# Optimization experiments

Measured on AMD Instinct MI355X. Metric: run time of the kernel, lower is better.

The kernel has to match this reference:

```python
import jax, jax.numpy as jnp
import numpy as np

NU = 100000
NV = 100000
EF = 500000
EB = 500000
D = 64  # e_in = u_in = v_in = e_out = 64; u_out = v_out = 64 -> nu_dim = nv_dim = 32
DC = D + D  # concat dim: node_in + e_in = 128


def _lin(key, din, dout):
    kw, kb = jax.random.split(key)
    lim = 1.0 / np.sqrt(din)
    W = jax.random.uniform(kw, (din, dout), jnp.float32, -lim, lim)
    b = jax.random.uniform(kb, (dout,), jnp.float32, -lim, lim)
    return W, b


def setup_inputs() -> dict:
    key = jax.random.key(0)
    ks = jax.random.split(key, 20)
    inp = {
        'f_feat': jax.random.normal(ks[0], (EF, D), jnp.float32),
        'b_feat': jax.random.normal(ks[1], (EB, D), jnp.float32),
        'u_feat': jax.random.normal(ks[2], (NU, D), jnp.float32),
        'v_feat': jax.random.normal(ks[3], (NV, D), jnp.float32),
        'fsrc': jax.random.randint(ks[4], (EF,), 0, NU, jnp.int32),
        'fdst': jax.random.randint(ks[5], (EF,), 0, NV, jnp.int32),
        'bsrc': jax.random.randint(ks[6], (EB,), 0, NV, jnp.int32),
        'bdst': jax.random.randint(ks[7], (EB,), 0, NU, jnp.int32),
    }
    inp['We'], inp['be'] = _lin(ks[8], D, D)        # e_linear
    inp['Wul'], inp['bul'] = _lin(ks[9], D, D)      # u_linear
    inp['Wvl'], inp['bvl'] = _lin(ks[10], D, D)     # v_linear
    inp['Wau'], inp['bau'] = _lin(ks[11], D, DC)    # W_ATTN_u: u_in -> v_in+e_in
    inp['Wav'], inp['bav'] = _lin(ks[12], D, DC)    # W_ATTN_v: v_in -> u_in+e_in
    inp['Wwu'], inp['bwu'] = _lin(ks[13], DC, D // 2)  # W_u
    inp['Wwv'], inp['bwv'] = _lin(ks[14], DC, D // 2)  # W_v
    inp['WVu'], inp['bVu'] = _lin(ks[15], D, D - D // 2)  # Vu
    inp['WVv'], inp['bVv'] = _lin(ks[16], D, D - D // 2)  # Vv
    return inp


def _edge_softmax(scores, dst, n):
    # scores: [E,1]; softmax over edges grouped by destination node
    m = jax.ops.segment_max(scores, dst, num_segments=n)
    e = jnp.exp(scores - m[dst])
    s = jax.ops.segment_sum(e, dst, num_segments=n)
    return e / s[dst]


def reference(f_feat, b_feat, u_feat, v_feat, fsrc, fdst, bsrc, bdst,
              We, be, Wul, bul, Wvl, bvl, Wau, bau, Wav, bav,
              Wwu, bwu, Wwv, bwv, WVu, bVu, WVv, bVv):
    Nu, Nv = u_feat.shape[0], v_feat.shape[0]
    he_u = u_feat @ Wul + bul
    he_v = v_feat @ Wvl + bvl
    # edge hidden: he_e + he of incident u and v (activation is None, dropout 0)
    hf = f_feat @ We + be + he_u[fsrc] + he_v[fdst]   # forward: src=u, dst=v
    hb = b_feat @ We + be + he_v[bsrc] + he_u[bdst]   # backward: src=v, dst=u
    # concat raw src node feat with raw edge feat
    h_ue = jnp.concatenate([u_feat[fsrc], f_feat], axis=-1)  # [EF, DC]
    h_ve = jnp.concatenate([v_feat[bsrc], b_feat], axis=-1)  # [EB, DC]
    att_u = u_feat @ Wau + bau  # [Nu, DC]
    att_v = v_feat @ Wav + bav  # [Nv, DC]
    s_f = jnp.sum(h_ue * att_v[fdst], axis=-1, keepdims=True)  # e_dot_v
    s_b = jnp.sum(h_ve * att_u[bdst], axis=-1, keepdims=True)
    sfm_f = _edge_softmax(s_f, fdst, Nv)
    sfm_b = _edge_softmax(s_b, bdst, Nu)
    agg_v = jax.ops.segment_sum(h_ue * sfm_f, fdst, num_segments=Nv)
    agg_u = jax.ops.segment_sum(h_ve * sfm_b, bdst, num_segments=Nu)
    h_nu = agg_u @ Wwu + bwu
    h_nv = agg_v @ Wwv + bwv
    hu = jnp.concatenate([u_feat @ WVu + bVu, h_nu], axis=-1)
    hv = jnp.concatenate([v_feat @ WVv + bVv, h_nv], axis=-1)
    return hf, hb, hu, hv
```

## Files before the change

kernel.cpp:

```cpp
#include <hip/hip_runtime.h>
#include <hip/hip_bf16.h>
#include <cstdint>

typedef __attribute__((ext_vector_type(4))) float f32x4;
typedef __attribute__((ext_vector_type(8))) short bf16x8;

__device__ inline unsigned short f2bf(float f) {
    union { float f; unsigned u; } v; v.f = f;
    unsigned r = v.u + 0x7FFFu + ((v.u >> 16) & 1u);
    return (unsigned short)(r >> 16);
}
__device__ inline float bf2f(unsigned short h) {
    union { unsigned u; float f; } v; v.u = ((unsigned)h) << 16;
    return v.f;
}

__global__ void prep_kernel(
    const float* __restrict__ We,
    const float* __restrict__ Wul, const float* __restrict__ Wau, const float* __restrict__ WVu,
    const float* __restrict__ Wvl, const float* __restrict__ Wav, const float* __restrict__ WVv,
    const float* __restrict__ Wwu, const float* __restrict__ Wwv,
    const float* __restrict__ bul, const float* __restrict__ bau, const float* __restrict__ bVu,
    const float* __restrict__ bvl, const float* __restrict__ bav, const float* __restrict__ bVv,
    unsigned short* __restrict__ WeXf, unsigned short* __restrict__ WeXb,
    unsigned short* __restrict__ WnTu, unsigned short* __restrict__ WnTv,
    float* __restrict__ bcu, float* __restrict__ bcv)
{
    int tid0 = blockIdx.x * blockDim.x + threadIdx.x;
    int stride = gridDim.x * blockDim.x;
    for (int i = tid0; i < 176 * 64; i += stride) {
        int c = i >> 6, k = i & 63;
        float vf, vb;
        if (c < 64)       { vf = We[k * 64 + c];               vb = vf; }
        else if (c < 96)  { vf = Wwv[(64 + k) * 32 + (c - 64)]; vb = Wwu[(64 + k) * 32 + (c - 64)]; }
        else if (c < 160) { vf = Wav[(c - 96) * 128 + 64 + k];  vb = Wau[(c - 96) * 128 + 64 + k]; }
        else if (c == 160){ vf = bav[64 + k];                   vb = bau[64 + k]; }
        else              { vf = 0.f;                           vb = 0.f; }
        WeXf[i] = f2bf(vf);
        WeXb[i] = f2bf(vb);
    }
    for (int i = tid0; i < 208 * 64; i += stride) {
        int c = i >> 6, k = i & 63;
        float vu, vv;
        if (c < 64)       { vu = Wul[k * 64 + c];           vv = Wvl[k * 64 + c]; }
        else if (c < 128) { vu = Wav[(c - 64) * 128 + k];   vv = Wau[(c - 64) * 128 + k]; }
        else if (c < 160) { vu = WVu[k * 32 + (c - 128)];   vv = WVv[k * 32 + (c - 128)]; }
        else if (c < 192) { vu = Wwv[k * 32 + (c - 160)];   vv = Wwu[k * 32 + (c - 160)]; }
        else if (c == 192){ vu = bav[k];                    vv = bau[k]; }
        else              { vu = 0.f;                       vv = 0.f; }
        WnTu[i] = f2bf(vu);
        WnTv[i] = f2bf(vv);
    }
    for (int i = tid0; i < 208; i += stride) {
        float u = 0.f, v = 0.f;
        if (i < 64)                { u = bul[i];       v = bvl[i]; }
        else if (i >= 128 && i < 160) { u = bVu[i - 128]; v = bVv[i - 128]; }
        bcu[i] = u; bcv[i] = v;
    }
}

__global__ __launch_bounds__(256, 4) void node_pre_kernel(
    int nbU, int NU, int NV,
    const float* __restrict__ featU, const float* __restrict__ featV,
    const unsigned short* __restrict__ WTu, const unsigned short* __restrict__ WTv,
    const float* __restrict__ bcu, const float* __restrict__ bcv,
    unsigned short* __restrict__ heU, unsigned short* __restrict__ heV,
    unsigned short* __restrict__ ztU, unsigned short* __restrict__ ztV,
    unsigned short* __restrict__ nbfU, unsigned short* __restrict__ nbfV,
    float* __restrict__ outU, float* __restrict__ outV,
    float* __restrict__ projU, float* __restrict__ projV,
    float* __restrict__ sbU, float* __restrict__ sbV,
    float* __restrict__ aggU, float* __restrict__ aggV,
    float* __restrict__ wsU, float* __restrict__ wsV)
{
    bool isu = (int)blockIdx.x < nbU;
    int blk = isu ? blockIdx.x : blockIdx.x - nbU;
    int N = isu ? NU : NV;
    const float* feat = isu ? featU : featV;
    const unsigned short* WT = isu ? WTu : WTv;
    const float* bc = isu ? bcu : bcv;
    unsigned short* he = isu ? heU : heV;
    unsigned short* zt = isu ? ztU : ztV;
    unsigned short* nbf = isu ? nbfU : nbfV;
    float* outp = isu ? outU : outV;
    float* proj = isu ? projU : projV;
    float* sb = isu ? sbU : sbV;
    float* agg32 = isu ? aggU : aggV;
    float* ws = isu ? wsU : wsV;

    __shared__ unsigned short lA[64 * 64];
    __shared__ unsigned short lW[208 * 64];
    int tid = threadIdx.x;
    int n0 = blk * 64;

    const uint4* wsrc = (const uint4*)WT;
    for (int i = tid; i < 208 * 8; i += 256) {
        int r = i >> 3, ch = i & 7;
        *(uint4*)&lW[r * 64 + ((ch ^ (r & 7)) << 3)] = wsrc[i];
    }
    #pragma unroll
    for (int j = 0; j < 4; ++j) {
        int fi = j * 1024 + tid * 4;
        int r = fi >> 6, k = fi & 63;
        int n = n0 + r;
        f32x4 v = (f32x4){0.f, 0.f, 0.f, 0.f};
        if (n < N) v = __builtin_nontemporal_load((const f32x4*)&feat[(size_t)n * 64 + k]);
        uint2 pk;
        pk.x = (unsigned)f2bf(v.x) | ((unsigned)f2bf(v.y) << 16);
        pk.y = (unsigned)f2bf(v.z) | ((unsigned)f2bf(v.w) << 16);
        *(uint2*)&lA[r * 64 + (((k >> 3) ^ (r & 7)) << 3) + (k & 7)] = pk;
        if (n < N) *(uint2*)&nbf[(size_t)n * 64 + k] = pk;
    }
    {
        for (int i = tid; i < 64 * 32; i += 256) {
            int n = n0 + (i >> 5);
            if (n < N) agg32[(size_t)n * 32 + (i & 31)] = 0.f;
        }
        if (tid < 64) { int n = n0 + tid; if (n < N) ws[n] = 0.f; }
    }
    __syncthreads();

    int wv = tid >> 6, lane = tid & 63;
    int r0 = wv * 16;
    int lrow = lane & 15, lkg = lane >> 4;
    int rr = r0 + lrow;

    bf16x8 a[2];
    #pragma unroll
    for (int h = 0; h < 2; ++h) {
        int ch = h * 4 + lkg;
        a[h] = *(const bf16x8*)&lA[rr * 64 + ((ch ^ (rr & 7)) << 3)];
    }
    f32x4 acc[13];
    #pragma unroll
    for (int t = 0; t < 13; ++t) acc[t] = (f32x4){0.f, 0.f, 0.f, 0.f};
    #pragma unroll
    for (int t = 0; t < 13; ++t) {
        int row = t * 16 + lrow;
        #pragma unroll
        for (int h = 0; h < 2; ++h) {
            int ch = h * 4 + lkg;
            bf16x8 b = *(const bf16x8*)&lW[row * 64 + ((ch ^ (row & 7)) << 3)];
            acc[t] = __builtin_amdgcn_mfma_f32_16x16x32_bf16(a[h], b, acc[t], 0, 0, 0);
        }
    }
    #pragma unroll
    for (int t = 0; t < 13; ++t) {
        #pragma unroll
        for (int q = 0; q < 4; ++q) {
            int n = n0 + r0 + lkg * 4 + q;
            if (n >= N) continue;
            int c = t * 16 + lrow;
            float raw = acc[t][q];
            if (t < 4) {
                he[(size_t)n * 64 + c] = f2bf(raw + bc[c]);
            } else if (t < 8) {
                zt[(size_t)n * 64 + (c - 64)] = f2bf(raw);
            } else if (t < 10) {
                __builtin_nontemporal_store(raw + bc[c], &outp[(size_t)n * 64 + (c - 128)]);
            } else if (t < 12) {
                proj[(size_t)n * 32 + (c - 160)] = raw;
            } else if (lrow == 0) {
                sb[n] = raw;
            }
        }
    }
}

__global__ __launch_bounds__(256, 5) void edge_kernel(
    int nbF, int EF, int EB,
    const float* __restrict__ efF, const float* __restrict__ efB,
    const int* __restrict__ srcF, const int* __restrict__ dstF,
    const int* __restrict__ srcB, const int* __restrict__ dstB,
    const unsigned short* __restrict__ zF, const unsigned short* __restrict__ zB,
    const float* __restrict__ sbF, const float* __restrict__ sbB,
    const float* __restrict__ projF, const float* __restrict__ projB,
    const unsigned short* __restrict__ heSF, const unsigned short* __restrict__ heSB,
    const unsigned short* __restrict__ heDF, const unsigned short* __restrict__ heDB,
    const unsigned short* __restrict__ nbfF, const unsigned short* __restrict__ nbfB,
    const unsigned short* __restrict__ WeXF, const unsigned short* __restrict__ WeXB,
    const float* __restrict__ be,
    float* __restrict__ outF, float* __restrict__ outB,
    float* __restrict__ aggF, float* __restrict__ aggB,
    float* __restrict__ wsF, float* __restrict__ wsB)
{
    bool fwd = (int)blockIdx.x < nbF;
    int blk = fwd ? blockIdx.x : blockIdx.x - nbF;
    int E = fwd ? EF : EB;
    const float* efeat = fwd ? efF : efB;
    const int* src = fwd ? srcF : srcB;
    const int* dst = fwd ? dstF : dstB;
    const unsigned short* z_src = fwd ? zF : zB;
    const float* sb_src = fwd ? sbF : sbB;
    const float* proj_src = fwd ? projF : projB;
    const unsigned short* he_src = fwd ? heSF : heSB;
    const unsigned short* he_dst = fwd ? heDF : heDB;
    const unsigned short* nbf_dst = fwd ? nbfF : nbfB;
    const unsigned short* WeX = fwd ? WeXF : WeXB;
    float* out_he = fwd ? outF : outB;
    float* agg32 = fwd ? aggF : aggB;
    float* wsum = fwd ? wsF : wsB;

    __shared__ unsigned short lW[176 * 64];
    int tid = threadIdx.x;
    int lane = tid & 63;
    int wvu = __builtin_amdgcn_readfirstlane(tid >> 6);
    int e0 = blk * 64;
    int eBase = e0 + wvu * 16;
    int lrow = lane & 15, lkg = lane >> 4;

    const uint4* wsrc = (const uint4*)WeX;
    for (int i = tid; i < 176 * 8; i += 256) {
        int r = i >> 3, ch = i & 7;
        *(uint4*)&lW[r * 64 + ((ch ^ (r & 7)) << 3)] = wsrc[i];
    }

    int sil[4], dil[4];
    #pragma unroll
    for (int j = 0; j < 4; ++j) {
        int e = eBase + lkg * 4 + j;
        sil[j] = (e < E) ? src[e] : 0;
        dil[j] = (e < E) ? dst[e] : 0;
    }

    int er = eBase + lrow;
    bool rok = er < E;
    const float* arow = &efeat[(size_t)er * 64];
    bf16x8 a[2];
    #pragma unroll
    for (int h = 0; h < 2; ++h) {
        int ch = h * 4 + lkg;
        f32x4 v0 = (f32x4){0.f, 0.f, 0.f, 0.f}, v1 = v0;
        if (rok) {
            v0 = *(const f32x4*)&arow[ch * 8];
            v1 = *(const f32x4*)&arow[ch * 8 + 4];
        }
        bf16x8 av;
        av[0] = (short)f2bf(v0.x); av[1] = (short)f2bf(v0.y);
        av[2] = (short)f2bf(v0.z); av[3] = (short)f2bf(v0.w);
        av[4] = (short)f2bf(v1.x); av[5] = (short)f2bf(v1.y);
        av[6] = (short)f2bf(v1.z); av[7] = (short)f2bf(v1.w);
        a[h] = av;
    }
    __syncthreads();

    f32x4 acc[11];
    #pragma unroll
    for (int t = 0; t < 11; ++t) acc[t] = (f32x4){0.f, 0.f, 0.f, 0.f};
    #pragma unroll
    for (int t = 0; t < 11; ++t) {
        int row = t * 16 + lrow;
        #pragma unroll
        for (int h = 0; h < 2; ++h) {
            int ch = h * 4 + lkg;
            bf16x8 b = *(const bf16x8*)&lW[row * 64 + ((ch ^ (row & 7)) << 3)];
            acc[t] = __builtin_amdgcn_mfma_f32_16x16x32_bf16(a[h], b, acc[t], 0, 0, 0);
        }
    }

    float wq[4];
    #pragma unroll
    for (int j = 0; j < 4; ++j) {
        int e = eBase + lkg * 4 + j;
        float p = acc[10][j];
        if (e < E) {
            int si = sil[j], di = dil[j];
            const unsigned short* zr = &z_src[(size_t)si * 64 + lrow];
            const unsigned short* vr = &nbf_dst[(size_t)di * 64 + lrow];
            #pragma unroll
            for (int tt = 0; tt < 4; ++tt) {
                float zv = bf2f(zr[tt * 16]) + acc[6 + tt][j];
                p += zv * bf2f(vr[tt * 16]);
            }
            if (lrow == 1) p += sb_src[si];
        }
        p += __shfl_xor(p, 1, 64);
        p += __shfl_xor(p, 2, 64);
        p += __shfl_xor(p, 4, 64);
        p += __shfl_xor(p, 8, 64);
        wq[j] = __expf(p);
    }

    #pragma unroll
    for (int j = 0; j < 4; ++j) {
        int e = eBase + lkg * 4 + j;
        if (e >= E) continue;
        float w = wq[j];
        int si = sil[j], di = dil[j];
        #pragma unroll
        for (int h = 0; h < 2; ++h) {
            int c = lrow + h * 16;
            float pv = proj_src[(size_t)si * 32 + c] + acc[4 + h][j];
            unsafeAtomicAdd(&agg32[(size_t)di * 32 + c], w * pv);
        }
        if (lrow == 2) unsafeAtomicAdd(&wsum[di], w);
    }

    float bev[4];
    #pragma unroll
    for (int t = 0; t < 4; ++t) bev[t] = be[t * 16 + lrow];
    #pragma unroll
    for (int q = 0; q < 4; ++q) {
        int e = eBase + lkg * 4 + q;
        if (e >= E) continue;
        int si = sil[q], di = dil[q];
        #pragma unroll
        for (int t = 0; t < 4; ++t) {
            int c = t * 16 + lrow;
            float hs = bf2f(he_src[(size_t)si * 64 + c]);
            float hd = bf2f(he_dst[(size_t)di * 64 + c]);
            __builtin_nontemporal_store(acc[t][q] + bev[t] + hs + hd,
                                        &out_he[(size_t)e * 64 + c]);
        }
    }
}

__global__ void finalize_kernel(const float* __restrict__ aggU, const float* __restrict__ wsU,
                                const float* __restrict__ aggV, const float* __restrict__ wsV,
                                int NU, int NV,
                                const float* __restrict__ bwu, const float* __restrict__ bwv,
                                float* __restrict__ outU, float* __restrict__ outV)
{
    int idx = blockIdx.x * blockDim.x + threadIdx.x;
    int tot = (NU + NV) * 32;
    if (idx >= tot) return;
    bool isu = idx < NU * 32;
    int li = isu ? idx : idx - NU * 32;
    int n = li >> 5, c = li & 31;
    const float* agg = isu ? aggU : aggV;
    const float* ws = isu ? wsU : wsV;
    const float* bias = isu ? bwu : bwv;
    float* outp = isu ? outU : outV;
    float s = ws[n];
    float sc = (s > 0.f) ? 1.0f / s : 0.f;
    __builtin_nontemporal_store(agg[li] * sc + bias[c], &outp[(size_t)n * 64 + 32 + c]);
}

extern "C" void kernel_launch(void* const* d_in, const int* in_sizes, int n_in,
                              void* d_out, int out_size, void* d_ws, size_t ws_size,
                              hipStream_t stream)
{
    const float* f_feat = (const float*)d_in[0];
    const float* b_feat = (const float*)d_in[1];
    const float* u_feat = (const float*)d_in[2];
    const float* v_feat = (const float*)d_in[3];
    const int* fsrc = (const int*)d_in[4];
    const int* fdst = (const int*)d_in[5];
    const int* bsrc = (const int*)d_in[6];
    const int* bdst = (const int*)d_in[7];
    const float* We  = (const float*)d_in[8];
    const float* be  = (const float*)d_in[9];
    const float* Wul = (const float*)d_in[10];
    const float* bul = (const float*)d_in[11];
    const float* Wvl = (const float*)d_in[12];
    const float* bvl = (const float*)d_in[13];
    const float* Wau = (const float*)d_in[14];
    const float* bau = (const float*)d_in[15];
    const float* Wav = (const float*)d_in[16];
    const float* bav = (const float*)d_in[17];
    const float* Wwu = (const float*)d_in[18];
    const float* bwu = (const float*)d_in[19];
    const float* Wwv = (const float*)d_in[20];
    const float* bwv = (const float*)d_in[21];
    const float* WVu = (const float*)d_in[22];
    const float* bVu = (const float*)d_in[23];
    const float* WVv = (const float*)d_in[24];
    const float* bVv = (const float*)d_in[25];

    int EF = in_sizes[0] / 64;
    int EB = in_sizes[1] / 64;
    int NU = in_sizes[2] / 64;
    int NV = in_sizes[3] / 64;

    float* out = (float*)d_out;
    float* hf = out;
    float* hb = hf + (size_t)EF * 64;
    float* hu = hb + (size_t)EB * 64;
    float* hv = hu + (size_t)NU * 64;

    char* wp = (char*)d_ws;
    auto alloc = [&](size_t bytes) { char* p = wp; wp += (bytes + 255) & ~(size_t)255; return p; };
    unsigned short* he_u  = (unsigned short*)alloc((size_t)NU * 64 * 2);
    unsigned short* he_v  = (unsigned short*)alloc((size_t)NV * 64 * 2);
    unsigned short* z_u   = (unsigned short*)alloc((size_t)NU * 64 * 2);
    unsigned short* z_v   = (unsigned short*)alloc((size_t)NV * 64 * 2);
    unsigned short* nbf_u = (unsigned short*)alloc((size_t)NU * 64 * 2);
    unsigned short* nbf_v = (unsigned short*)alloc((size_t)NV * 64 * 2);
    float* proj_u = (float*)alloc((size_t)NU * 32 * 4);
    float* proj_v = (float*)alloc((size_t)NV * 32 * 4);
    float* sb_u   = (float*)alloc((size_t)NU * 4);
    float* sb_v   = (float*)alloc((size_t)NV * 4);
    float* agg_u  = (float*)alloc((size_t)NU * 32 * 4);
    float* agg_v  = (float*)alloc((size_t)NV * 32 * 4);
    float* ws_u   = (float*)alloc((size_t)NU * 4);
    float* ws_v   = (float*)alloc((size_t)NV * 4);
    unsigned short* WeXf = (unsigned short*)alloc(176 * 64 * 2);
    unsigned short* WeXb = (unsigned short*)alloc(176 * 64 * 2);
    unsigned short* WnTu = (unsigned short*)alloc(208 * 64 * 2);
    unsigned short* WnTv = (unsigned short*)alloc(208 * 64 * 2);
    float* bcu = (float*)alloc(208 * 4);
    float* bcv = (float*)alloc(208 * 4);

    prep_kernel<<<64, 256, 0, stream>>>(We, Wul, Wau, WVu, Wvl, Wav, WVv, Wwu, Wwv,
                                        bul, bau, bVu, bvl, bav, bVv,
                                        WeXf, WeXb, WnTu, WnTv, bcu, bcv);

    int nbU = (NU + 63) / 64, nbV = (NV + 63) / 64;
    node_pre_kernel<<<nbU + nbV, 256, 0, stream>>>(nbU, NU, NV, u_feat, v_feat,
                                                   WnTu, WnTv, bcu, bcv,
                                                   he_u, he_v, z_u, z_v, nbf_u, nbf_v,
                                                   hu, hv, proj_u, proj_v, sb_u, sb_v,
                                                   agg_u, agg_v, ws_u, ws_v);

    int nbF = (EF + 63) / 64, nbB = (EB + 63) / 64;
    edge_kernel<<<nbF + nbB, 256, 0, stream>>>(nbF, EF, EB, f_feat, b_feat,
                                               fsrc, fdst, bsrc, bdst,
                                               z_u, z_v, sb_u, sb_v, proj_u, proj_v,
                                               he_u, he_v, he_v, he_u,
                                               nbf_v, nbf_u,
                                               WeXf, WeXb, be,
                                               hf, hb, agg_v, agg_u, ws_v, ws_u);

    finalize_kernel<<<((NU + NV) * 32 + 255) / 256, 256, 0, stream>>>(
        agg_u, ws_u, agg_v, ws_v, NU, NV, bwu, bwv, hu, hv);
}
```

Before: 357.7 us.

## Permute node-side bf16 tables so edge gathers read four contiguous values per lane

Node tables he, z and nbf are now stored with a column permutation (lrow*4+t), so each edge-kernel lane gathers its four values with one 8-byte load instead of four strided 2-byte loads. To write nbf in that permuted layout, the node kernel appends an identity block to the weight matrix and produces nbf through MFMA, and it loads features straight into registers instead of staging them in LDS. The edge kernel's feature loads become nontemporal. In exchange the node kernel does about 30% more MFMA work and uses more registers.

```diff
diff --git a/kernel.cpp b/kernel.cpp
--- a/kernel.cpp
+++ b/kernel.cpp
@@ -4,6 +4,7 @@
 
 typedef __attribute__((ext_vector_type(4))) float f32x4;
 typedef __attribute__((ext_vector_type(8))) short bf16x8;
+typedef __attribute__((ext_vector_type(4))) unsigned short u16x4;
 
 __device__ inline unsigned short f2bf(float f) {
     union { float f; unsigned u; } v; v.f = f;
@@ -39,7 +40,7 @@
         WeXf[i] = f2bf(vf);
         WeXb[i] = f2bf(vb);
     }
-    for (int i = tid0; i < 208 * 64; i += stride) {
+    for (int i = tid0; i < 272 * 64; i += stride) {
         int c = i >> 6, k = i & 63;
         float vu, vv;
         if (c < 64)       { vu = Wul[k * 64 + c];           vv = Wvl[k * 64 + c]; }
@@ -47,7 +48,8 @@
         else if (c < 160) { vu = WVu[k * 32 + (c - 128)];   vv = WVv[k * 32 + (c - 128)]; }
         else if (c < 192) { vu = Wwv[k * 32 + (c - 160)];   vv = Wwu[k * 32 + (c - 160)]; }
         else if (c == 192){ vu = bav[k];                    vv = bau[k]; }
-        else              { vu = 0.f;                       vv = 0.f; }
+        else if (c < 208) { vu = 0.f;                       vv = 0.f; }
+        else              { vu = (k == c - 208) ? 1.f : 0.f; vv = vu; }
         WnTu[i] = f2bf(vu);
         WnTv[i] = f2bf(vv);
     }
@@ -88,28 +90,14 @@
     float* agg32 = isu ? aggU : aggV;
     float* ws = isu ? wsU : wsV;
 
-    __shared__ unsigned short lA[64 * 64];
-    __shared__ unsigned short lW[208 * 64];
+    __shared__ unsigned short lW[272 * 64];
     int tid = threadIdx.x;
     int n0 = blk * 64;
 
     const uint4* wsrc = (const uint4*)WT;
-    for (int i = tid; i < 208 * 8; i += 256) {
+    for (int i = tid; i < 272 * 8; i += 256) {
         int r = i >> 3, ch = i & 7;
         *(uint4*)&lW[r * 64 + ((ch ^ (r & 7)) << 3)] = wsrc[i];
-    }
-    #pragma unroll
-    for (int j = 0; j < 4; ++j) {
-        int fi = j * 1024 + tid * 4;
-        int r = fi >> 6, k = fi & 63;
-        int n = n0 + r;
-        f32x4 v = (f32x4){0.f, 0.f, 0.f, 0.f};
-        if (n < N) v = __builtin_nontemporal_load((const f32x4*)&feat[(size_t)n * 64 + k]);
-        uint2 pk;
-        pk.x = (unsigned)f2bf(v.x) | ((unsigned)f2bf(v.y) << 16);
-        pk.y = (unsigned)f2bf(v.z) | ((unsigned)f2bf(v.w) << 16);
-        *(uint2*)&lA[r * 64 + (((k >> 3) ^ (r & 7)) << 3) + (k & 7)] = pk;
-        if (n < N) *(uint2*)&nbf[(size_t)n * 64 + k] = pk;
     }
     {
         for (int i = tid; i < 64 * 32; i += 256) {
@@ -118,24 +106,37 @@
         }
         if (tid < 64) { int n = n0 + tid; if (n < N) ws[n] = 0.f; }
     }
-    __syncthreads();
 
     int wv = tid >> 6, lane = tid & 63;
     int r0 = wv * 16;
     int lrow = lane & 15, lkg = lane >> 4;
-    int rr = r0 + lrow;
-
+
+    int nr = n0 + r0 + lrow;
+    bool rok = nr < N;
+    const float* arow = &feat[(size_t)nr * 64];
     bf16x8 a[2];
     #pragma unroll
     for (int h = 0; h < 2; ++h) {
         int ch = h * 4 + lkg;
-        a[h] = *(const bf16x8*)&lA[rr * 64 + ((ch ^ (rr & 7)) << 3)];
-    }
-    f32x4 acc[13];
-    #pragma unroll
-    for (int t = 0; t < 13; ++t) acc[t] = (f32x4){0.f, 0.f, 0.f, 0.f};
-    #pragma unroll
-    for (int t = 0; t < 13; ++t) {
+        f32x4 v0 = (f32x4){0.f, 0.f, 0.f, 0.f}, v1 = v0;
+        if (rok) {
+            v0 = __builtin_nontemporal_load((const f32x4*)&arow[ch * 8]);
+            v1 = __builtin_nontemporal_load((const f32x4*)&arow[ch * 8 + 4]);
+        }
+        bf16x8 av;
+        av[0] = (short)f2bf(v0.x); av[1] = (short)f2bf(v0.y);
+        av[2] = (short)f2bf(v0.z); av[3] = (short)f2bf(v0.w);
+        av[4] = (short)f2bf(v1.x); av[5] = (short)f2bf(v1.y);
+        av[6] = (short)f2bf(v1.z); av[7] = (short)f2bf(v1.w);
+        a[h] = av;
+    }
+    __syncthreads();
+
+    f32x4 acc[17];
+    #pragma unroll
+    for (int t = 0; t < 17; ++t) acc[t] = (f32x4){0.f, 0.f, 0.f, 0.f};
+    #pragma unroll
+    for (int t = 0; t < 17; ++t) {
         int row = t * 16 + lrow;
         #pragma unroll
         for (int h = 0; h < 2; ++h) {
@@ -145,7 +146,7 @@
         }
     }
     #pragma unroll
-    for (int t = 0; t < 13; ++t) {
+    for (int t = 0; t < 17; ++t) {
         #pragma unroll
         for (int q = 0; q < 4; ++q) {
             int n = n0 + r0 + lkg * 4 + q;
@@ -153,15 +154,17 @@
             int c = t * 16 + lrow;
             float raw = acc[t][q];
             if (t < 4) {
-                he[(size_t)n * 64 + c] = f2bf(raw + bc[c]);
+                he[(size_t)n * 64 + lrow * 4 + t] = f2bf(raw + bc[c]);
             } else if (t < 8) {
-                zt[(size_t)n * 64 + (c - 64)] = f2bf(raw);
+                zt[(size_t)n * 64 + lrow * 4 + (t - 4)] = f2bf(raw);
             } else if (t < 10) {
                 __builtin_nontemporal_store(raw + bc[c], &outp[(size_t)n * 64 + (c - 128)]);
             } else if (t < 12) {
                 proj[(size_t)n * 32 + (c - 160)] = raw;
-            } else if (lrow == 0) {
-                sb[n] = raw;
+            } else if (t == 12) {
+                if (lrow == 0) sb[n] = raw;
+            } else {
+                nbf[(size_t)n * 64 + lrow * 4 + (t - 13)] = f2bf(raw);
             }
         }
     }
@@ -232,8 +235,8 @@
         int ch = h * 4 + lkg;
         f32x4 v0 = (f32x4){0.f, 0.f, 0.f, 0.f}, v1 = v0;
         if (rok) {
-            v0 = *(const f32x4*)&arow[ch * 8];
-            v1 = *(const f32x4*)&arow[ch * 8 + 4];
+            v0 = __builtin_nontemporal_load((const f32x4*)&arow[ch * 8]);
+            v1 = __builtin_nontemporal_load((const f32x4*)&arow[ch * 8 + 4]);
         }
         bf16x8 av;
         av[0] = (short)f2bf(v0.x); av[1] = (short)f2bf(v0.y);
@@ -265,12 +268,12 @@
         float p = acc[10][j];
         if (e < E) {
             int si = sil[j], di = dil[j];
-            const unsigned short* zr = &z_src[(size_t)si * 64 + lrow];
-            const unsigned short* vr = &nbf_dst[(size_t)di * 64 + lrow];
+            u16x4 zr = *(const u16x4*)&z_src[(size_t)si * 64 + lrow * 4];
+            u16x4 vr = *(const u16x4*)&nbf_dst[(size_t)di * 64 + lrow * 4];
             #pragma unroll
             for (int tt = 0; tt < 4; ++tt) {
-                float zv = bf2f(zr[tt * 16]) + acc[6 + tt][j];
-                p += zv * bf2f(vr[tt * 16]);
+                float zv = bf2f(zr[tt]) + acc[6 + tt][j];
+                p += zv * bf2f(vr[tt]);
             }
             if (lrow == 1) p += sb_src[si];
         }
@@ -304,12 +307,12 @@
         int e = eBase + lkg * 4 + q;
         if (e >= E) continue;
         int si = sil[q], di = dil[q];
+        u16x4 hs4 = *(const u16x4*)&he_src[(size_t)si * 64 + lrow * 4];
+        u16x4 hd4 = *(const u16x4*)&he_dst[(size_t)di * 64 + lrow * 4];
         #pragma unroll
         for (int t = 0; t < 4; ++t) {
             int c = t * 16 + lrow;
-            float hs = bf2f(he_src[(size_t)si * 64 + c]);
-            float hd = bf2f(he_dst[(size_t)di * 64 + c]);
-            __builtin_nontemporal_store(acc[t][q] + bev[t] + hs + hd,
+            __builtin_nontemporal_store(acc[t][q] + bev[t] + bf2f(hs4[t]) + bf2f(hd4[t]),
                                         &out_he[(size_t)e * 64 + c]);
         }
     }
@@ -396,8 +399,8 @@
     float* ws_v   = (float*)alloc((size_t)NV * 4);
     unsigned short* WeXf = (unsigned short*)alloc(176 * 64 * 2);
     unsigned short* WeXb = (unsigned short*)alloc(176 * 64 * 2);
-    unsigned short* WnTu = (unsigned short*)alloc(208 * 64 * 2);
-    unsigned short* WnTv = (unsigned short*)alloc(208 * 64 * 2);
+    unsigned short* WnTu = (unsigned short*)alloc(272 * 64 * 2);
+    unsigned short* WnTv = (unsigned short*)alloc(272 * 64 * 2);
     float* bcu = (float*)alloc(208 * 4);
     float* bcv = (float*)alloc(208 * 4);
 
```

Result: faster. 350.1 us (-2.1%).
